# Kernel tuning notes

Hardware: AMD Instinct MI355X
Metric: run time of the kernel (lower is better)

## Reference

```python
import jax, jax.numpy as jnp
import numpy as np

CLASSES = 5

def setup_inputs() -> dict:
    key = jax.random.key(0)
    k1, k2, k3, k4 = jax.random.split(key, 4)
    B, C, H, Wd = 4, 128, 256, 256
    MS = 8
    image = jax.random.normal(k1, (B, C, H, Wd), dtype=jnp.float32)
    clusters = jax.random.randint(k2, (B, 1, H, Wd), 0, CLASSES, dtype=jnp.int64)
    # nn.Linear-style init: U(-1/sqrt(fan_in), 1/sqrt(fan_in))
    bound = 1.0 / np.sqrt(C)
    W = jax.random.uniform(k3, (CLASSES, MS, C), minval=-bound, maxval=bound, dtype=jnp.float32)
    b = jax.random.uniform(k4, (CLASSES, MS), minval=-bound, maxval=bound, dtype=jnp.float32)
    return {"image": image, "clusters": clusters, "W": W, "b": b}

def reference(image, clusters, W, b):
    # image: [B, C, H, W]; clusters: [B, 1, H, W] with labels in [0, CLASSES)
    # Per-pixel: out = relu(x @ W_l^T + b_l) where l = cluster label of that pixel.
    x = jnp.transpose(image, (0, 2, 3, 1))              # [B, H, W, C]
    # Dense per-class linear + relu: [B, H, W, L, M]
    all_out = jax.nn.relu(jnp.einsum('bhwc,lmc->bhwlm', x, W) + b)
    labels = clusters[:, 0]                              # [B, H, W]
    sel = jnp.take_along_axis(all_out, labels[..., None, None], axis=3)[..., 0, :]  # [B,H,W,M]
    # Pixels with label >= CLASSES would remain zero in the original; randint keeps all in range.
    valid = (labels >= 0) & (labels < CLASSES)
    sel = jnp.where(valid[..., None], sel, 0.0)
    return jnp.transpose(sel, (0, 3, 1, 2))              # [B, M, H, W]
```

## Files before the change

### kernel.cpp

```cpp
#include <hip/hip_runtime.h>

#define NCLASSES 5
#define MS 8
#define NC 128
#define HW (256 * 256)

__global__ __launch_bounds__(256, 4) void clusterdown_kernel(
    const float* __restrict__ image,
    const int* __restrict__ clusters,
    const float* __restrict__ Wg,
    const float* __restrict__ bg,
    float* __restrict__ out,
    int n_pix)
{
    __shared__ float wlds[NC * NCLASSES * MS];
    __shared__ float blds[NCLASSES * MS];

    const int tid = threadIdx.x;

    for (int i = tid; i < NCLASSES * MS * NC; i += 256) {
        int l = i / (MS * NC);
        int r = i - l * (MS * NC);
        int m = r / NC;
        int c = r - m * NC;
        wlds[(c * NCLASSES + l) * MS + m] = Wg[i];
    }
    if (tid < NCLASSES * MS) blds[tid] = bg[tid];
    __syncthreads();

    const int p = blockIdx.x * 256 + tid;
    if (p >= n_pix) return;

    const int bidx = p / HW;
    const int hw   = p - bidx * HW;

    const int lab = clusters[p];
    const bool valid = (lab >= 0) && (lab < NCLASSES);
    const int l = valid ? lab : 0;

    float acc[MS];
#pragma unroll
    for (int m = 0; m < MS; ++m) acc[m] = blds[l * MS + m];

    const float* ip = image + (size_t)bidx * NC * HW + hw;

#pragma unroll 8
    for (int c = 0; c < NC; ++c) {
        const float v = ip[(size_t)c * HW];
        const float4* wp = (const float4*)&wlds[(c * NCLASSES + l) * MS];
        const float4 w0 = wp[0];
        const float4 w1 = wp[1];
        acc[0] = fmaf(v, w0.x, acc[0]);
        acc[1] = fmaf(v, w0.y, acc[1]);
        acc[2] = fmaf(v, w0.z, acc[2]);
        acc[3] = fmaf(v, w0.w, acc[3]);
        acc[4] = fmaf(v, w1.x, acc[4]);
        acc[5] = fmaf(v, w1.y, acc[5]);
        acc[6] = fmaf(v, w1.z, acc[6]);
        acc[7] = fmaf(v, w1.w, acc[7]);
    }

    float* op = out + (size_t)bidx * MS * HW + hw;
#pragma unroll
    for (int m = 0; m < MS; ++m) {
        const float r = valid ? fmaxf(acc[m], 0.0f) : 0.0f;
        op[(size_t)m * HW] = r;
    }
}

extern "C" void kernel_launch(void* const* d_in, const int* in_sizes, int n_in,
                              void* d_out, int out_size, void* d_ws, size_t ws_size,
                              hipStream_t stream) {
    const float* image    = (const float*)d_in[0];
    const int* clusters   = (const int*)d_in[1];
    const float* Wg       = (const float*)d_in[2];
    const float* bg       = (const float*)d_in[3];
    float* out            = (float*)d_out;

    const int n_pix = in_sizes[1];
    const int block = 256;
    const int grid  = (n_pix + block - 1) / block;

    clusterdown_kernel<<<grid, block, 0, stream>>>(image, clusters, Wg, bg, out, n_pix);
}
```

Baseline: 28.52 us.

## Process two pixels per thread with float2 loads and software-prefetched channels

Each thread now handles two adjacent pixels, loading image channels, labels and writing outputs as float2/int2 vectors. The channel loop is fully unrolled and keeps four channel loads in flight ahead of use, a manual prefetch pipeline. This halves the grid and aims for wider memory transactions and more memory-level parallelism. The cost is higher register pressure (launch bounds lowered to 2 waves per SIMD) and fewer blocks, each of which still pays for filling the weight table in LDS.

New measurement: 29.44 us. 3.2% more time.

```diff
diff --git a/kernel.cpp b/kernel.cpp
--- a/kernel.cpp
+++ b/kernel.cpp
@@ -4,8 +4,34 @@
 #define MS 8
 #define NC 128
 #define HW (256 * 256)
+#define PPT 2
 
-__global__ __launch_bounds__(256, 4) void clusterdown_kernel(
+
+#define STAGE(v, c)                                                          \
+    do {                                                                     \
+        const float4* wp0 = (const float4*)&wlds[((c) * NCLASSES + l0) * MS];\
+        const float4 a0 = wp0[0], a1 = wp0[1];                               \
+        const float4* wp1 = (const float4*)&wlds[((c) * NCLASSES + l1) * MS];\
+        const float4 b0 = wp1[0], b1 = wp1[1];                               \
+        acc0[0] = fmaf(v.x, a0.x, acc0[0]);                                  \
+        acc0[1] = fmaf(v.x, a0.y, acc0[1]);                                  \
+        acc0[2] = fmaf(v.x, a0.z, acc0[2]);                                  \
+        acc0[3] = fmaf(v.x, a0.w, acc0[3]);                                  \
+        acc0[4] = fmaf(v.x, a1.x, acc0[4]);                                  \
+        acc0[5] = fmaf(v.x, a1.y, acc0[5]);                                  \
+        acc0[6] = fmaf(v.x, a1.z, acc0[6]);                                  \
+        acc0[7] = fmaf(v.x, a1.w, acc0[7]);                                  \
+        acc1[0] = fmaf(v.y, b0.x, acc1[0]);                                  \
+        acc1[1] = fmaf(v.y, b0.y, acc1[1]);                                  \
+        acc1[2] = fmaf(v.y, b0.z, acc1[2]);                                  \
+        acc1[3] = fmaf(v.y, b0.w, acc1[3]);                                  \
+        acc1[4] = fmaf(v.y, b1.x, acc1[4]);                                  \
+        acc1[5] = fmaf(v.y, b1.y, acc1[5]);                                  \
+        acc1[6] = fmaf(v.y, b1.z, acc1[6]);                                  \
+        acc1[7] = fmaf(v.y, b1.w, acc1[7]);                                  \
+    } while (0)
+
+__global__ __launch_bounds__(256, 2) void clusterdown_kernel(
     const float* __restrict__ image,
     const int* __restrict__ clusters,
     const float* __restrict__ Wg,
@@ -28,58 +54,68 @@
     if (tid < NCLASSES * MS) blds[tid] = bg[tid];
     __syncthreads();
 
-    const int p = blockIdx.x * 256 + tid;
-    if (p >= n_pix) return;
+    const int t = blockIdx.x * 256 + tid;
+    const int base = t * PPT;
+    if (base >= n_pix) return;
 
-    const int bidx = p / HW;
-    const int hw   = p - bidx * HW;
+    const int bidx = base / HW;
+    const int hw   = base - bidx * HW;
 
-    const int lab = clusters[p];
-    const bool valid = (lab >= 0) && (lab < NCLASSES);
-    const int l = valid ? lab : 0;
+    const int2 lab2 = *(const int2*)&clusters[base];
+    const bool valid0 = (lab2.x >= 0) && (lab2.x < NCLASSES);
+    const bool valid1 = (lab2.y >= 0) && (lab2.y < NCLASSES);
+    const int l0 = valid0 ? lab2.x : 0;
+    const int l1 = valid1 ? lab2.y : 0;
 
-    float acc[MS];
+    float acc0[MS], acc1[MS];
 #pragma unroll
-    for (int m = 0; m < MS; ++m) acc[m] = blds[l * MS + m];
+    for (int m = 0; m < MS; ++m) {
+        acc0[m] = blds[l0 * MS + m];
+        acc1[m] = blds[l1 * MS + m];
+    }
 
     const float* ip = image + (size_t)bidx * NC * HW + hw;
 
-#pragma unroll 8
-    for (int c = 0; c < NC; ++c) {
-        const float v = ip[(size_t)c * HW];
-        const float4* wp = (const float4*)&wlds[(c * NCLASSES + l) * MS];
-        const float4 w0 = wp[0];
-        const float4 w1 = wp[1];
-        acc[0] = fmaf(v, w0.x, acc[0]);
-        acc[1] = fmaf(v, w0.y, acc[1]);
-        acc[2] = fmaf(v, w0.z, acc[2]);
-        acc[3] = fmaf(v, w0.w, acc[3]);
-        acc[4] = fmaf(v, w1.x, acc[4]);
-        acc[5] = fmaf(v, w1.y, acc[5]);
-        acc[6] = fmaf(v, w1.z, acc[6]);
-        acc[7] = fmaf(v, w1.w, acc[7]);
+    float2 v0 = *(const float2*)&ip[(size_t)0 * HW];
+    float2 v1 = *(const float2*)&ip[(size_t)1 * HW];
+    float2 v2 = *(const float2*)&ip[(size_t)2 * HW];
+    float2 v3 = *(const float2*)&ip[(size_t)3 * HW];
+
+#pragma unroll
+    for (int cc = 0; cc < NC; cc += 4) {
+        STAGE(v0, cc + 0);
+        if (cc + 4 < NC) v0 = *(const float2*)&ip[(size_t)(cc + 4) * HW];
+        STAGE(v1, cc + 1);
+        if (cc + 5 < NC) v1 = *(const float2*)&ip[(size_t)(cc + 5) * HW];
+        STAGE(v2, cc + 2);
+        if (cc + 6 < NC) v2 = *(const float2*)&ip[(size_t)(cc + 6) * HW];
+        STAGE(v3, cc + 3);
+        if (cc + 7 < NC) v3 = *(const float2*)&ip[(size_t)(cc + 7) * HW];
     }
 
     float* op = out + (size_t)bidx * MS * HW + hw;
 #pragma unroll
     for (int m = 0; m < MS; ++m) {
-        const float r = valid ? fmaxf(acc[m], 0.0f) : 0.0f;
-        op[(size_t)m * HW] = r;
+        float2 r;
+        r.x = valid0 ? fmaxf(acc0[m], 0.0f) : 0.0f;
+        r.y = valid1 ? fmaxf(acc1[m], 0.0f) : 0.0f;
+        *(float2*)&op[(size_t)m * HW] = r;
     }
 }
 
 extern "C" void kernel_launch(void* const* d_in, const int* in_sizes, int n_in,
                               void* d_out, int out_size, void* d_ws, size_t ws_size,
                               hipStream_t stream) {
-    const float* image    = (const float*)d_in[0];
-    const int* clusters   = (const int*)d_in[1];
-    const float* Wg       = (const float*)d_in[2];
-    const float* bg       = (const float*)d_in[3];
-    float* out            = (float*)d_out;
+    const float* image  = (const float*)d_in[0];
+    const int* clusters = (const int*)d_in[1];
+    const float* Wg     = (const float*)d_in[2];
+    const float* bg     = (const float*)d_in[3];
+    float* out          = (float*)d_out;
 
-    const int n_pix = in_sizes[1];
-    const int block = 256;
-    const int grid  = (n_pix + block - 1) / block;
+    const int n_pix   = in_sizes[1];
+    const int threads = n_pix / PPT;
+    const int block   = 256;
+    const int grid    = (threads + block - 1) / block;
 
     clusterdown_kernel<<<grid, block, 0, stream>>>(image, clusters, Wg, bg, out, n_pix);
 }
```
